# Performance work log

Measured on AMD Instinct MI355X. Metric: run time of the kernel, lower is better.

## Reference

```python
import jax, jax.numpy as jnp
import numpy as np

B, N, C = 1, 6400, 256
NUM_CAMS, NUM_HEADS, NUM_LEVELS, NUM_POINTS = 6, 8, 3, 8
LVL_SHAPES = [(64, 176), (32, 88), (16, 44)]
IMG_H, IMG_W = 512, 1408


def setup_inputs():
    key = jax.random.key(0)
    ks = jax.random.split(key, 16)
    # Gaussian means in ego frame: depth z in [2,40]; x/y scaled so projections land in-image
    z = jax.random.uniform(ks[0], (B, N, 1), minval=2.0, maxval=40.0)
    xy = jax.random.uniform(ks[1], (B, N, 2), minval=-0.5, maxval=0.5)
    means = jnp.concatenate([xy[..., 0:1] * z * 0.8, xy[..., 1:2] * z * 0.4, z], -1)
    feature = jax.random.normal(ks[2], (B, N, C)) * 0.5
    feat0 = jax.random.normal(ks[3], (B * NUM_CAMS, C, 64, 176)) * 0.5
    feat1 = jax.random.normal(ks[4], (B * NUM_CAMS, C, 32, 88)) * 0.5
    feat2 = jax.random.normal(ks[5], (B * NUM_CAMS, C, 16, 44)) * 0.5
    cam2ego = jnp.tile(jnp.eye(4), (B, NUM_CAMS, 1, 1))
    cam2ego = cam2ego.at[..., :3, 3].set(jax.random.uniform(ks[6], (B, NUM_CAMS, 3), minval=-0.5, maxval=0.5))
    intrins = jnp.tile(jnp.array([[500., 0., 704.], [0., 500., 256.], [0., 0., 1.]]), (B, NUM_CAMS, 1, 1))
    post_rots = jnp.tile(jnp.eye(3), (B, NUM_CAMS, 1, 1))
    post_trans = jnp.concatenate([jax.random.uniform(ks[7], (B, NUM_CAMS, 2), minval=-30., maxval=30.),
                                  jnp.zeros((B, NUM_CAMS, 1))], -1)
    # deformable-attn style bias init for sampling offsets (as in init_weights)
    thetas = np.arange(NUM_HEADS) * (2.0 * np.pi / NUM_HEADS)
    grid = np.stack([np.cos(thetas), np.sin(thetas)], -1)
    grid = grid / np.abs(grid).max(-1, keepdims=True)
    grid = np.tile(grid.reshape(NUM_HEADS, 1, 1, 2), (1, NUM_LEVELS, NUM_POINTS, 1))
    grid = grid * (np.arange(NUM_POINTS) + 1).reshape(1, 1, NUM_POINTS, 1)
    b_off = jnp.asarray(grid.reshape(-1), jnp.float32)
    W_off = jax.random.normal(ks[8], (C, NUM_HEADS * NUM_LEVELS * NUM_POINTS * 2)) * 0.01
    W_attn = jax.random.normal(ks[9], (C, NUM_HEADS * NUM_LEVELS * NUM_POINTS)) * 0.02
    b_attn = jnp.zeros((NUM_HEADS * NUM_LEVELS * NUM_POINTS,))
    W_val = jax.random.normal(ks[10], (C, C)) * (1.0 / np.sqrt(C))
    b_val = jnp.zeros((C,))
    W_out = jax.random.normal(ks[11], (C, C)) * (1.0 / np.sqrt(C))
    b_out = jnp.zeros((C,))
    cams_embeds = jax.random.normal(ks[12], (NUM_CAMS, C))
    level_embeds = jax.random.normal(ks[13], (NUM_LEVELS, C))
    ln_g = jnp.ones((C,))
    ln_b = jnp.zeros((C,))
    return dict(means=means, feature=feature, feat0=feat0, feat1=feat1, feat2=feat2,
                cam2ego=cam2ego, intrins=intrins, post_rots=post_rots, post_trans=post_trans,
                W_off=W_off, b_off=b_off, W_attn=W_attn, b_attn=b_attn, W_val=W_val, b_val=b_val,
                W_out=W_out, b_out=b_out, cams_embeds=cams_embeds, level_embeds=level_embeds,
                ln_g=ln_g, ln_b=ln_b, img_h=IMG_H, img_w=IMG_W)


def _msda(value, shapes, loc, attn):
    # Multi-scale deformable attention (matches multi_scale_deformable_attn_pytorch,
    # i.e. grid_sample bilinear, align_corners=False, zero padding).
    # value [Bc,S,H,D]; loc [Bc,Nq,H,L,P,2] in [0,1]; attn [Bc,Nq,H,L,P]
    Bc, S, Hh, D = value.shape
    Nq, P = loc.shape[1], loc.shape[4]
    out = jnp.zeros((Bc, Hh, Nq, D), value.dtype)
    start = 0
    for lvl, (h, w) in enumerate(shapes):
        v = value[:, start:start + h * w].transpose(0, 2, 1, 3)  # [Bc,H,h*w,D]
        l = loc[:, :, :, lvl]                                    # [Bc,Nq,H,P,2]
        x = l[..., 0] * w - 0.5  # align_corners=False pixel coords
        y = l[..., 1] * h - 0.5
        x0 = jnp.floor(x)
        y0 = jnp.floor(y)
        tx = x - x0
        ty = y - y0
        a = attn[:, :, :, lvl]                                   # [Bc,Nq,H,P]
        def samp(xi, yi, wgt):
            valid = (xi >= 0) & (xi <= w - 1) & (yi >= 0) & (yi <= h - 1)
            idx = (jnp.clip(yi, 0, h - 1) * w + jnp.clip(xi, 0, w - 1)).astype(jnp.int32)
            idx = idx.transpose(0, 2, 1, 3).reshape(Bc, Hh, Nq * P)
            g = jnp.take_along_axis(v, idx[..., None], axis=2)   # [Bc,H,Nq*P,D]
            coef = wgt * jnp.where(valid, 1.0, 0.0).astype(v.dtype) * a
            return g * coef.transpose(0, 2, 1, 3).reshape(Bc, Hh, Nq * P, 1)
        acc = (samp(x0, y0, (1 - tx) * (1 - ty)) + samp(x0 + 1, y0, tx * (1 - ty))
               + samp(x0, y0 + 1, (1 - tx) * ty) + samp(x0 + 1, y0 + 1, tx * ty))
        out = out + acc.reshape(Bc, Hh, Nq, P, D).sum(3)
        start += h * w
    return out.transpose(0, 2, 1, 3).reshape(Bc, Nq, Hh * D)


def reference(means, feature, feat0, feat1, feat2, cam2ego, intrins, post_rots, post_trans,
              W_off, b_off, W_attn, b_attn, W_val, b_val, W_out, b_out,
              cams_embeds, level_embeds, ln_g, ln_b, img_h, img_w):
    Bq, Nq, Cc = feature.shape
    D = Cc // NUM_HEADS
    # --- project reference points into each camera (project_reference_points) ---
    mh = jnp.concatenate([means, jnp.ones((Bq, Nq, 1), means.dtype)], -1)      # [B,N,4]
    means_cam = jnp.einsum('bcij,bnj->bcni', jnp.linalg.inv(cam2ego), mh)[..., :3]
    means_img = jnp.einsum('bcij,bcnj->bcni', intrins, means_cam)              # [B,cams,N,3]
    mi = jnp.concatenate([means_img[..., :2] / (means_img[..., 2:] + 1e-4), means_img[..., 2:]], -1)
    mi = jnp.einsum('bcij,bcnj->bcni', post_rots, mi) + post_trans[:, :, None, :]
    coor = mi[..., :2] / jnp.array([img_w, img_h], feature.dtype)              # [B,cams,N,2]
    depth = mi[..., 2]
    mask = ((depth > 0.01) & (coor[..., 0] > 0.) & (coor[..., 0] < 1.)
            & (coor[..., 1] > 0.) & (coor[..., 1] < 1.))                        # [B,cams,N]
    # --- per-query sampling offsets / attention weights (shared across cameras) ---
    offsets = (feature @ W_off + b_off).reshape(Bq, Nq, NUM_HEADS, NUM_LEVELS, NUM_POINTS, 2)
    attn = jax.nn.softmax((feature @ W_attn + b_attn).reshape(Bq, Nq, NUM_HEADS, NUM_LEVELS * NUM_POINTS), -1)
    attn = attn.reshape(Bq, Nq, NUM_HEADS, NUM_LEVELS, NUM_POINTS)
    # --- flatten multi-level feats + cam/level embeds, value projection ---
    feats = (feat0, feat1, feat2)
    shapes = [(f.shape[2], f.shape[3]) for f in feats]
    flat = []
    for lvl, f in enumerate(feats):
        h, w = shapes[lvl]
        fl = f.reshape(Bq, NUM_CAMS, Cc, h * w)
        fl = fl + cams_embeds[None, :, :, None] + level_embeds[lvl][None, None, :, None]
        flat.append(fl)
    value = jnp.concatenate(flat, -1).transpose(0, 1, 3, 2).reshape(Bq * NUM_CAMS, -1, Cc)
    value = (value @ W_val + b_val).reshape(Bq * NUM_CAMS, -1, NUM_HEADS, D)
    # --- sampling locations per camera ---
    norm = jnp.array([[w, h] for (h, w) in shapes], feature.dtype)             # [L,2] = (W_l,H_l)
    loc = coor[:, :, :, None, None, None, :] + offsets[:, None] / norm[None, None, None, None, :, None, :]
    loc = loc.reshape(Bq * NUM_CAMS, Nq, NUM_HEADS, NUM_LEVELS, NUM_POINTS, 2)
    attn_bc = jnp.broadcast_to(attn[:, None], (Bq, NUM_CAMS, Nq, NUM_HEADS, NUM_LEVELS, NUM_POINTS))
    attn_bc = attn_bc.reshape(Bq * NUM_CAMS, Nq, NUM_HEADS, NUM_LEVELS, NUM_POINTS)
    out = _msda(value, shapes, loc, attn_bc).reshape(Bq, NUM_CAMS, Nq, Cc)
    # --- mask-weighted combine over cameras (mathematically equals the rebatch/scatter) ---
    mf = mask.astype(feature.dtype)
    slots = (out * mf[..., None]).sum(1) / jnp.maximum(mf.sum(1), 1.0)[..., None]
    slots = slots @ W_out + b_out
    x = slots + feature  # dropout is identity at inference
    mu = jnp.mean(x, -1, keepdims=True)
    var = jnp.mean((x - mu) ** 2, -1, keepdims=True)
    return (x - mu) / jnp.sqrt(var + 1e-5) * ln_g + ln_b
```

## Files before the change

### kernel.cpp

```cpp
#include <hip/hip_runtime.h>
#include <hip/hip_bf16.h>

typedef __bf16 bf16;
typedef __attribute__((ext_vector_type(4))) float f32x4;
typedef __attribute__((ext_vector_type(8))) bf16 bf16x8;
typedef __attribute__((ext_vector_type(2))) bf16 bf16x2;

#define NCAMS 6
#define NQ 6400
#define CH 256
#define NH 8
#define NL 3
#define NP 8
#define S_TOT 14784

#if __has_builtin(__builtin_amdgcn_fdot2_f32_bf16) && __has_builtin(__builtin_amdgcn_perm)
#define MSDA_DOT2 1
#else
#define MSDA_DOT2 0
#endif

__global__ __launch_bounds__(256) void k_prep(
    const float* __restrict__ means, const float* __restrict__ cam2ego,
    const float* __restrict__ intrins, const float* __restrict__ post_rots,
    const float* __restrict__ post_trans, const int* __restrict__ img_h,
    const int* __restrict__ img_w,
    const float* __restrict__ W_val, const float* __restrict__ W_off,
    const float* __restrict__ W_attn, const float* __restrict__ W_out,
    float* __restrict__ coor, float* __restrict__ maskf,
    bf16* __restrict__ Wvp, bf16* __restrict__ Woap, bf16* __restrict__ Wop)
{
    int bid = blockIdx.x;
    if (bid < 150) {
        int idx = bid * 256 + threadIdx.x;
        if (idx >= NCAMS * NQ) return;
        int cam = idx / NQ, n = idx % NQ;
        float mx = means[n*3+0], my = means[n*3+1], mz = means[n*3+2];
        const float* M = cam2ego + cam*16;
        float R[3][3], t[3];
        #pragma unroll
        for (int r = 0; r < 3; r++) {
            #pragma unroll
            for (int c = 0; c < 3; c++) R[r][c] = M[r*4+c];
            t[r] = M[r*4+3];
        }
        float dx = mx - t[0], dy = my - t[1], dz = mz - t[2];
        float xc = R[0][0]*dx + R[1][0]*dy + R[2][0]*dz;
        float yc = R[0][1]*dx + R[1][1]*dy + R[2][1]*dz;
        float zc = R[0][2]*dx + R[1][2]*dy + R[2][2]*dz;
        const float* K = intrins + cam*9;
        float ix = K[0]*xc + K[1]*yc + K[2]*zc;
        float iy = K[3]*xc + K[4]*yc + K[5]*zc;
        float iz = K[6]*xc + K[7]*yc + K[8]*zc;
        float px = ix / (iz + 1e-4f), py = iy / (iz + 1e-4f), pz = iz;
        const float* P = post_rots + cam*9;
        const float* T = post_trans + cam*3;
        float vx = P[0]*px + P[1]*py + P[2]*pz + T[0];
        float vy = P[3]*px + P[4]*py + P[5]*pz + T[1];
        float vz = P[6]*px + P[7]*py + P[8]*pz + T[2];
        float cx = vx / (float)img_w[0];
        float cy = vy / (float)img_h[0];
        bool ok = (vz > 0.01f) && (cx > 0.f) && (cx < 1.f) && (cy > 0.f) && (cy < 1.f);
        coor[idx*2+0] = cx;
        coor[idx*2+1] = cy;
        maskf[idx] = ok ? 1.f : 0.f;
        return;
    }
    int flat = (bid - 150) * 256 + threadIdx.x;
    if (flat < 8192) {
        int kc = flat >> 10, rem = flat & 1023;
        int nf = rem >> 6, lane = rem & 63;
        int q = lane >> 4, col = nf*16 + (lane & 15);
        bf16x8 v;
        #pragma unroll
        for (int j = 0; j < 8; j++) v[j] = (bf16)W_val[(size_t)(kc*32 + q*8 + j)*256 + col];
        *reinterpret_cast<bf16x8*>(Wvp + (size_t)flat*8) = v;
    } else if (flat < 26624) {
        int f2 = flat - 8192;
        int kc = f2 / (36*64), rem = f2 % (36*64);
        int nf = rem >> 6, lane = rem & 63;
        int q = lane >> 4, col = nf*16 + (lane & 15);
        bf16x8 v;
        #pragma unroll
        for (int j = 0; j < 8; j++) {
            int k = kc*32 + q*8 + j;
            float x = (col < 384) ? W_off[(size_t)k*384 + col] : W_attn[(size_t)k*192 + (col-384)];
            v[j] = (bf16)x;
        }
        *reinterpret_cast<bf16x8*>(Woap + (size_t)f2*8) = v;
    } else if (flat < 34816) {
        int f3 = flat - 26624;
        int kc = f3 >> 10, rem = f3 & 1023;
        int nf = rem >> 6, lane = rem & 63;
        int q = lane >> 4, col = nf*16 + (lane & 15);
        bf16x8 v;
        #pragma unroll
        for (int j = 0; j < 8; j++) v[j] = (bf16)W_out[(size_t)(kc*32 + q*8 + j)*256 + col];
        *reinterpret_cast<bf16x8*>(Wop + (size_t)f3*8) = v;
    }
}

__global__ __launch_bounds__(256) void k_mid(
    const float* __restrict__ feature, const bf16* __restrict__ Woap,
    const float* __restrict__ b_off, const float* __restrict__ b_attn,
    float* __restrict__ offs, bf16* __restrict__ attn_out,
    const float* __restrict__ f0, const float* __restrict__ f1, const float* __restrict__ f2,
    const float* __restrict__ cams_embeds, const float* __restrict__ level_embeds,
    const bf16* __restrict__ Wvp, const float* __restrict__ b_val, bf16* __restrict__ value)
{
    __shared__ alignas(16) char smem[14336];
    int t = threadIdx.x, lane = t & 63, w = t >> 6;
    int q = lane >> 4, r16 = lane & 15;

    if (blockIdx.x < 400) {
        float (*lg)[200] = reinterpret_cast<float(*)[200]>(smem);
        int n0 = blockIdx.x * 16;

        f32x4 acc[9];
        #pragma unroll
        for (int i = 0; i < 9; i++) acc[i] = (f32x4){0.f,0.f,0.f,0.f};

        const float* arow = feature + (size_t)(n0 + r16)*CH;
        for (int kc = 0; kc < 8; kc++) {
            f32x4 a0 = *reinterpret_cast<const f32x4*>(arow + kc*32 + q*8);
            f32x4 a1 = *reinterpret_cast<const f32x4*>(arow + kc*32 + q*8 + 4);
            bf16x8 afr;
            #pragma unroll
            for (int i = 0; i < 4; i++) { afr[i] = (bf16)a0[i]; afr[4+i] = (bf16)a1[i]; }
            #pragma unroll
            for (int nf9 = 0; nf9 < 9; nf9++) {
                bf16x8 bfr = *reinterpret_cast<const bf16x8*>(Woap + ((size_t)(kc*36 + w*9 + nf9)*64 + lane)*8);
                acc[nf9] = __builtin_amdgcn_mfma_f32_16x16x32_bf16(afr, bfr, acc[nf9], 0, 0, 0);
            }
        }
        #pragma unroll
        for (int nf9 = 0; nf9 < 9; nf9++) {
            int nfg = w*9 + nf9;
            int nglob = nfg*16 + r16;
            if (nfg < 24) {
                float bias = b_off[nglob];
                #pragma unroll
                for (int r = 0; r < 4; r++)
                    offs[(size_t)(n0 + q*4 + r)*384 + nglob] = acc[nf9][r] + bias;
            } else {
                int la = nglob - 384;
                float bias = b_attn[la];
                #pragma unroll
                for (int r = 0; r < 4; r++)
                    lg[q*4 + r][la] = acc[nf9][r] + bias;
            }
        }
        __syncthreads();
        if (t < 128) {
            int m = t >> 3, h = t & 7;
            const float* L = &lg[m][h*24];
            float mx = -1e30f;
            #pragma unroll
            for (int j = 0; j < 24; j++) mx = fmaxf(mx, L[j]);
            float e[24]; float s = 0.f;
            #pragma unroll
            for (int j = 0; j < 24; j++) { e[j] = __expf(L[j] - mx); s += e[j]; }
            float inv = 1.f / s;
            #pragma unroll
            for (int j = 0; j < 24; j++) attn_out[(size_t)(n0+m)*192 + h*24 + j] = (bf16)(e[j]*inv);
        }
        return;
    }

    bf16 (*A)[48]    = reinterpret_cast<bf16(*)[48]>(smem);
    bf16 (*Cst)[256] = reinterpret_cast<bf16(*)[256]>(smem + 6144);
    int bi = blockIdx.x - 400;
    int cam = bi / 231, mb = bi % 231;
    int lvl, local0, HW;
    const float* fp;
    if (mb < 176)      { lvl = 0; local0 = mb*64;        fp = f0; HW = 11264; }
    else if (mb < 220) { lvl = 1; local0 = (mb-176)*64;  fp = f1; HW = 2816;  }
    else               { lvl = 2; local0 = (mb-220)*64;  fp = f2; HW = 704;   }
    int pos0 = (lvl == 0 ? 0 : (lvl == 1 ? 11264 : 14080)) + local0;
    const float* featbase = fp + (size_t)cam*CH*HW + local0;

    int kk = t >> 3;
    int m8 = (t & 7) * 8;

    f32x4 acc[4][4];
    #pragma unroll
    for (int i = 0; i < 4; i++)
        #pragma unroll
        for (int j = 0; j < 4; j++) acc[i][j] = (f32x4){0.f,0.f,0.f,0.f};

    for (int kc = 0; kc < 8; kc++) {
        __syncthreads();
        int kg = kc*32 + kk;
        float e = cams_embeds[cam*CH + kg] + level_embeds[lvl*CH + kg];
        f32x4 v0 = *reinterpret_cast<const f32x4*>(featbase + (size_t)kg*HW + m8);
        f32x4 v1 = *reinterpret_cast<const f32x4*>(featbase + (size_t)kg*HW + m8 + 4);
        #pragma unroll
        for (int i = 0; i < 4; i++) A[m8+i][kk]   = (bf16)(v0[i] + e);
        #pragma unroll
        for (int i = 0; i < 4; i++) A[m8+4+i][kk] = (bf16)(v1[i] + e);
        __syncthreads();

        bf16x8 bfr[4];
        #pragma unroll
        for (int nf = 0; nf < 4; nf++) {
            int nfg = w*4 + nf;
            bfr[nf] = *reinterpret_cast<const bf16x8*>(Wvp + ((size_t)(kc*16 + nfg)*64 + lane)*8);
        }
        #pragma unroll
        for (int mf = 0; mf < 4; mf++) {
            bf16x8 afr = *reinterpret_cast<const bf16x8*>(&A[mf*16 + r16][q*8]);
            #pragma unroll
            for (int nf = 0; nf < 4; nf++)
                acc[mf][nf] = __builtin_amdgcn_mfma_f32_16x16x32_bf16(afr, bfr[nf], acc[mf][nf], 0, 0, 0);
        }
    }
    int orow = t >> 4;
    int ocol = (t & 15) * 16;
    int ohead = ocol >> 5, och = ocol & 31;
    #pragma unroll
    for (int mf = 0; mf < 4; mf++) {
        __syncthreads();
        #pragma unroll
        for (int nf = 0; nf < 4; nf++) {
            int c = w*64 + nf*16 + r16;
            float bv = b_val[c];
            #pragma unroll
            for (int r = 0; r < 4; r++)
                Cst[q*4 + r][c] = (bf16)(acc[mf][nf][r] + bv);
        }
        __syncthreads();
        int srow = pos0 + mf*16 + orow;
        bf16* dst = value + ((size_t)(cam*NH + ohead)*S_TOT + srow)*32 + och;
        const f32x4* src = reinterpret_cast<const f32x4*>(&Cst[orow][ocol]);
        f32x4 x0 = src[0], x1 = src[1];
        reinterpret_cast<f32x4*>(dst)[0] = x0;
        reinterpret_cast<f32x4*>(dst)[1] = x1;
    }
}

__global__ __launch_bounds__(256) void k_msda(
    const float* __restrict__ coor, const float* __restrict__ offs,
    const bf16* __restrict__ attn, const bf16* __restrict__ value,
    const float* __restrict__ maskf, float* __restrict__ slots)
{
    __shared__ int4  s_o[NCAMS*192];
#if MSDA_DOT2
    __shared__ uint2 s_w[NCAMS*192];
#else
    __shared__ f32x4 s_w[NCAMS*192];
#endif
    int n = blockIdx.x;
    int t = threadIdx.x;

    for (int it = t; it < NCAMS*192; it += 256) {
        int cam = it / 192;
        int r   = it - cam*192;
        int hh  = r / 24;
        int rr  = r - hh*24;
        int lvl = rr >> 3;

        float mk = maskf[cam*NQ + n];
        float cx = coor[(cam*NQ + n)*2 + 0];
        float cy = coor[(cam*NQ + n)*2 + 1];
        float2 o2 = *reinterpret_cast<const float2*>(offs + (size_t)n*384 + r*2);
        float aw = (float)attn[(size_t)n*192 + r] * mk;

        int wi   = (lvl == 0) ? 176 : ((lvl == 1) ? 88 : 44);
        int hi   = (lvl == 0) ? 64  : ((lvl == 1) ? 32 : 16);
        int base = (lvl == 0) ? 0   : ((lvl == 1) ? 11264 : 14080);

        float x = cx*(float)wi + o2.x - 0.5f;
        float y = cy*(float)hi + o2.y - 0.5f;
        float xf = floorf(x), yf = floorf(y);
        float tx = x - xf, ty = y - yf;
        float wm1x = (float)(wi-1), wm1y = (float)(hi-1);
        bool vx0 = (xf >= 0.f)      && (xf <= wm1x);
        bool vx1 = (xf+1.f >= 0.f)  && (xf+1.f <= wm1x);
        bool vy0 = (yf >= 0.f)      && (yf <= wm1y);
        bool vy1 = (yf+1.f >= 0.f)  && (yf+1.f <= wm1y);
        int x0 = (int)fminf(fmaxf(xf,      0.f), wm1x);
        int x1 = (int)fminf(fmaxf(xf+1.f,  0.f), wm1x);
        int y0 = (int)fminf(fmaxf(yf,      0.f), wm1y);
        int y1 = (int)fminf(fmaxf(yf+1.f,  0.f), wm1y);
        float w00 = (1.f-tx)*(1.f-ty)*aw * ((vx0 && vy0) ? 1.f : 0.f);
        float w10 = tx*(1.f-ty)*aw       * ((vx1 && vy0) ? 1.f : 0.f);
        float w01 = (1.f-tx)*ty*aw       * ((vx0 && vy1) ? 1.f : 0.f);
        float w11 = tx*ty*aw             * ((vx1 && vy1) ? 1.f : 0.f);
        int rowb = (cam*NH + hh)*S_TOT + base;
        int r0 = rowb + y0*wi, r1 = rowb + y1*wi;
        s_o[it] = make_int4((r0 + x0)*64, (r0 + x1)*64, (r1 + x0)*64, (r1 + x1)*64);
#if MSDA_DOT2
        bf16x2 wa; wa[0] = (bf16)w00; wa[1] = (bf16)w10;
        bf16x2 wb; wb[0] = (bf16)w01; wb[1] = (bf16)w11;
        s_w[it] = make_uint2(__builtin_bit_cast(unsigned, wa),
                             __builtin_bit_cast(unsigned, wb));
#else
        s_w[it] = (f32x4){w00, w10, w01, w11};
#endif
    }
    __syncthreads();

    int lane = t & 63, wv = t >> 6;
    int hl = lane >> 5;
    int p  = (lane >> 2) & 7;
    int k2 = lane & 3;
    int hglob = wv*2 + hl;
    int kb = k2 * 16;
    int ibase = hglob*24 + p;

    f32x4 acc0 = (f32x4){0.f,0.f,0.f,0.f};
    f32x4 acc1 = (f32x4){0.f,0.f,0.f,0.f};
    const char* vbyte = (const char*)value;

    uint4 cA0,cA1,cA2, cB0,cB1,cB2, cC0,cC1,cC2, cD0,cD1,cD2;
#if MSDA_DOT2
    uint2 cw0, cw1, cw2;
#else
    f32x4 cw0, cw1, cw2;
#endif

#define LOADBATCH(CAMIDX, A0,A1,A2, B0,B1,B2, C0,C1,C2, D0,D1,D2, W0,W1,W2) \
    { int itb = (CAMIDX)*192 + ibase; \
      int4 o0 = s_o[itb]; int4 o1 = s_o[itb+8]; int4 o2v = s_o[itb+16]; \
      A0 = *reinterpret_cast<const uint4*>(vbyte + (o0.x + kb)); \
      B0 = *reinterpret_cast<const uint4*>(vbyte + (o0.y + kb)); \
      C0 = *reinterpret_cast<const uint4*>(vbyte + (o0.z + kb)); \
      D0 = *reinterpret_cast<const uint4*>(vbyte + (o0.w + kb)); \
      A1 = *reinterpret_cast<const uint4*>(vbyte + (o1.x + kb)); \
      B1 = *reinterpret_cast<const uint4*>(vbyte + (o1.y + kb)); \
      C1 = *reinterpret_cast<const uint4*>(vbyte + (o1.z + kb)); \
      D1 = *reinterpret_cast<const uint4*>(vbyte + (o1.w + kb)); \
      A2 = *reinterpret_cast<const uint4*>(vbyte + (o2v.x + kb)); \
      B2 = *reinterpret_cast<const uint4*>(vbyte + (o2v.y + kb)); \
      C2 = *reinterpret_cast<const uint4*>(vbyte + (o2v.z + kb)); \
      D2 = *reinterpret_cast<const uint4*>(vbyte + (o2v.w + kb)); \
      W0 = s_w[itb]; W1 = s_w[itb+8]; W2 = s_w[itb+16]; }

#if MSDA_DOT2
#define CONSUME1(d00, d10, d01, d11, WP) \
    { bf16x2 wa = __builtin_bit_cast(bf16x2, (WP).x); \
      bf16x2 wb = __builtin_bit_cast(bf16x2, (WP).y); \
      unsigned a0 = __builtin_amdgcn_perm((d10).x, (d00).x, 0x05040100u); \
      unsigned a1 = __builtin_amdgcn_perm((d10).x, (d00).x, 0x07060302u); \
      unsigned a2 = __builtin_amdgcn_perm((d10).y, (d00).y, 0x05040100u); \
      unsigned a3 = __builtin_amdgcn_perm((d10).y, (d00).y, 0x07060302u); \
      unsigned a4 = __builtin_amdgcn_perm((d10).z, (d00).z, 0x05040100u); \
      unsigned a5 = __builtin_amdgcn_perm((d10).z, (d00).z, 0x07060302u); \
      unsigned a6 = __builtin_amdgcn_perm((d10).w, (d00).w, 0x05040100u); \
      unsigned a7 = __builtin_amdgcn_perm((d10).w, (d00).w, 0x07060302u); \
      acc0[0] = __builtin_amdgcn_fdot2_f32_bf16(__builtin_bit_cast(bf16x2, a0), wa, acc0[0], false); \
      acc0[1] = __builtin_amdgcn_fdot2_f32_bf16(__builtin_bit_cast(bf16x2, a1), wa, acc0[1], false); \
      acc0[2] = __builtin_amdgcn_fdot2_f32_bf16(__builtin_bit_cast(bf16x2, a2), wa, acc0[2], false); \
      acc0[3] = __builtin_amdgcn_fdot2_f32_bf16(__builtin_bit_cast(bf16x2, a3), wa, acc0[3], false); \
      acc1[0] = __builtin_amdgcn_fdot2_f32_bf16(__builtin_bit_cast(bf16x2, a4), wa, acc1[0], false); \
      acc1[1] = __builtin_amdgcn_fdot2_f32_bf16(__builtin_bit_cast(bf16x2, a5), wa, acc1[1], false); \
      acc1[2] = __builtin_amdgcn_fdot2_f32_bf16(__builtin_bit_cast(bf16x2, a6), wa, acc1[2], false); \
      acc1[3] = __builtin_amdgcn_fdot2_f32_bf16(__builtin_bit_cast(bf16x2, a7), wa, acc1[3], false); \
      unsigned b0 = __builtin_amdgcn_perm((d11).x, (d01).x, 0x05040100u); \
      unsigned b1 = __builtin_amdgcn_perm((d11).x, (d01).x, 0x07060302u); \
      unsigned b2 = __builtin_amdgcn_perm((d11).y, (d01).y, 0x05040100u); \
      unsigned b3 = __builtin_amdgcn_perm((d11).y, (d01).y, 0x07060302u); \
      unsigned b4 = __builtin_amdgcn_perm((d11).z, (d01).z, 0x05040100u); \
      unsigned b5 = __builtin_amdgcn_perm((d11).z, (d01).z, 0x07060302u); \
      unsigned b6 = __builtin_amdgcn_perm((d11).w, (d01).w, 0x05040100u); \
      unsigned b7 = __builtin_amdgcn_perm((d11).w, (d01).w, 0x07060302u); \
      acc0[0] = __builtin_amdgcn_fdot2_f32_bf16(__builtin_bit_cast(bf16x2, b0), wb, acc0[0], false); \
      acc0[1] = __builtin_amdgcn_fdot2_f32_bf16(__builtin_bit_cast(bf16x2, b1), wb, acc0[1], false); \
      acc0[2] = __builtin_amdgcn_fdot2_f32_bf16(__builtin_bit_cast(bf16x2, b2), wb, acc0[2], false); \
      acc0[3] = __builtin_amdgcn_fdot2_f32_bf16(__builtin_bit_cast(bf16x2, b3), wb, acc0[3], false); \
      acc1[0] = __builtin_amdgcn_fdot2_f32_bf16(__builtin_bit_cast(bf16x2, b4), wb, acc1[0], false); \
      acc1[1] = __builtin_amdgcn_fdot2_f32_bf16(__builtin_bit_cast(bf16x2, b5), wb, acc1[1], false); \
      acc1[2] = __builtin_amdgcn_fdot2_f32_bf16(__builtin_bit_cast(bf16x2, b6), wb, acc1[2], false); \
      acc1[3] = __builtin_amdgcn_fdot2_f32_bf16(__builtin_bit_cast(bf16x2, b7), wb, acc1[3], false); }
#else
#define CONSUME1(d00, d10, d01, d11, WP) \
    { f32x4 w4 = (WP); \
      acc0[0] = fmaf(__uint_as_float((d00).x << 16),         w4.x, acc0[0]); \
      acc0[1] = fmaf(__uint_as_float((d00).x & 0xffff0000u), w4.x, acc0[1]); \
      acc0[2] = fmaf(__uint_as_float((d00).y << 16),         w4.x, acc0[2]); \
      acc0[3] = fmaf(__uint_as_float((d00).y & 0xffff0000u), w4.x, acc0[3]); \
      acc1[0] = fmaf(__uint_as_float((d00).z << 16),         w4.x, acc1[0]); \
      acc1[1] = fmaf(__uint_as_float((d00).z & 0xffff0000u), w4.x, acc1[1]); \
      acc1[2] = fmaf(__uint_as_float((d00).w << 16),         w4.x, acc1[2]); \
      acc1[3] = fmaf(__uint_as_float((d00).w & 0xffff0000u), w4.x, acc1[3]); \
      acc0[0] = fmaf(__uint_as_float((d10).x << 16),         w4.y, acc0[0]); \
      acc0[1] = fmaf(__uint_as_float((d10).x & 0xffff0000u), w4.y, acc0[1]); \
      acc0[2] = fmaf(__uint_as_float((d10).y << 16),         w4.y, acc0[2]); \
      acc0[3] = fmaf(__uint_as_float((d10).y & 0xffff0000u), w4.y, acc0[3]); \
      acc1[0] = fmaf(__uint_as_float((d10).z << 16),         w4.y, acc1[0]); \
      acc1[1] = fmaf(__uint_as_float((d10).z & 0xffff0000u), w4.y, acc1[1]); \
      acc1[2] = fmaf(__uint_as_float((d10).w << 16),         w4.y, acc1[2]); \
      acc1[3] = fmaf(__uint_as_float((d10).w & 0xffff0000u), w4.y, acc1[3]); \
      acc0[0] = fmaf(__uint_as_float((d01).x << 16),         w4.z, acc0[0]); \
      acc0[1] = fmaf(__uint_as_float((d01).x & 0xffff0000u), w4.z, acc0[1]); \
      acc0[2] = fmaf(__uint_as_float((d01).y << 16),         w4.z, acc0[2]); \
      acc0[3] = fmaf(__uint_as_float((d01).y & 0xffff0000u), w4.z, acc0[3]); \
      acc1[0] = fmaf(__uint_as_float((d01).z << 16),         w4.z, acc1[0]); \
      acc1[1] = fmaf(__uint_as_float((d01).z & 0xffff0000u), w4.z, acc1[1]); \
      acc1[2] = fmaf(__uint_as_float((d01).w << 16),         w4.z, acc1[2]); \
      acc1[3] = fmaf(__uint_as_float((d01).w & 0xffff0000u), w4.z, acc1[3]); \
      acc0[0] = fmaf(__uint_as_float((d11).x << 16),         w4.w, acc0[0]); \
      acc0[1] = fmaf(__uint_as_float((d11).x & 0xffff0000u), w4.w, acc0[1]); \
      acc0[2] = fmaf(__uint_as_float((d11).y << 16),         w4.w, acc0[2]); \
      acc0[3] = fmaf(__uint_as_float((d11).y & 0xffff0000u), w4.w, acc0[3]); \
      acc1[0] = fmaf(__uint_as_float((d11).z << 16),         w4.w, acc1[0]); \
      acc1[1] = fmaf(__uint_as_float((d11).z & 0xffff0000u), w4.w, acc1[1]); \
      acc1[2] = fmaf(__uint_as_float((d11).w << 16),         w4.w, acc1[2]); \
      acc1[3] = fmaf(__uint_as_float((d11).w & 0xffff0000u), w4.w, acc1[3]); }
#endif

    LOADBATCH(0, cA0,cA1,cA2, cB0,cB1,cB2, cC0,cC1,cC2, cD0,cD1,cD2, cw0,cw1,cw2)

    #pragma unroll
    for (int cam = 0; cam < NCAMS; cam++) {
        uint4 nA0,nA1,nA2, nB0,nB1,nB2, nC0,nC1,nC2, nD0,nD1,nD2;
#if MSDA_DOT2
        uint2 nw0, nw1, nw2;
#else
        f32x4 nw0, nw1, nw2;
#endif
        if (cam + 1 < NCAMS) {
            LOADBATCH(cam+1, nA0,nA1,nA2, nB0,nB1,nB2, nC0,nC1,nC2, nD0,nD1,nD2, nw0,nw1,nw2)
        }
        CONSUME1(cA0, cB0, cC0, cD0, cw0)
        CONSUME1(cA1, cB1, cC1, cD1, cw1)
        CONSUME1(cA2, cB2, cC2, cD2, cw2)
        if (cam + 1 < NCAMS) {
            cA0=nA0; cA1=nA1; cA2=nA2; cB0=nB0; cB1=nB1; cB2=nB2;
            cC0=nC0; cC1=nC1; cC2=nC2; cD0=nD0; cD1=nD1; cD2=nD2;
            cw0=nw0; cw1=nw1; cw2=nw2;
        }
    }
#undef LOADBATCH
#undef CONSUME1

    #pragma unroll
    for (int i = 0; i < 4; i++) {
        acc0[i] += __shfl_xor(acc0[i], 4);
        acc0[i] += __shfl_xor(acc0[i], 8);
        acc0[i] += __shfl_xor(acc0[i], 16);
        acc1[i] += __shfl_xor(acc1[i], 4);
        acc1[i] += __shfl_xor(acc1[i], 8);
        acc1[i] += __shfl_xor(acc1[i], 16);
    }
    if (p == 0) {
        float* dst = slots + (size_t)n*CH + hglob*32 + k2*8;
        *reinterpret_cast<f32x4*>(dst)     = acc0;
        *reinterpret_cast<f32x4*>(dst + 4) = acc1;
    }
}

__global__ __launch_bounds__(256) void k_final2(
    const float* __restrict__ slots, const float* __restrict__ maskf,
    const bf16* __restrict__ Wop, const float* __restrict__ b_out,
    const float* __restrict__ feature, const float* __restrict__ ln_g,
    const float* __restrict__ ln_b, float* __restrict__ out)
{
    __shared__ float yb[16][264];
    int t = threadIdx.x, lane = t & 63, w = t >> 6;
    int q = lane >> 4, r16 = lane & 15;
    int n0 = blockIdx.x * 16;

    float msum = 0.f;
    #pragma unroll
    for (int cam = 0; cam < NCAMS; cam++) msum += maskf[cam*NQ + n0 + r16];
    float inv = 1.f / fmaxf(msum, 1.f);

    f32x4 acc[4];
    #pragma unroll
    for (int i = 0; i < 4; i++) acc[i] = (f32x4){0.f,0.f,0.f,0.f};

    const float* srow = slots + (size_t)(n0 + r16)*CH;
    for (int kc = 0; kc < 8; kc++) {
        f32x4 a0 = *reinterpret_cast<const f32x4*>(srow + kc*32 + q*8);
        f32x4 a1 = *reinterpret_cast<const f32x4*>(srow + kc*32 + q*8 + 4);
        bf16x8 afr;
        #pragma unroll
        for (int i = 0; i < 4; i++) { afr[i] = (bf16)(a0[i]*inv); afr[4+i] = (bf16)(a1[i]*inv); }
        #pragma unroll
        for (int nf = 0; nf < 4; nf++) {
            bf16x8 bfr = *reinterpret_cast<const bf16x8*>(Wop + ((size_t)(kc*16 + w*4 + nf)*64 + lane)*8);
            acc[nf] = __builtin_amdgcn_mfma_f32_16x16x32_bf16(afr, bfr, acc[nf], 0, 0, 0);
        }
    }
    #pragma unroll
    for (int nf = 0; nf < 4; nf++) {
        int c = (w*4 + nf)*16 + r16;
        float bias = b_out[c];
        #pragma unroll
        for (int r = 0; r < 4; r++) {
            int m = q*4 + r;
            yb[m][c] = acc[nf][r] + bias + feature[(size_t)(n0+m)*CH + c];
        }
    }
    __syncthreads();
    int row = t >> 4, l16 = t & 15;
    int c0 = l16 * 16;
    float s = 0.f, s2 = 0.f;
    #pragma unroll
    for (int j = 0; j < 16; j++) {
        float v = yb[row][c0 + j];
        s += v; s2 += v*v;
    }
    #pragma unroll
    for (int off = 1; off < 16; off <<= 1) {
        s  += __shfl_xor(s, off);
        s2 += __shfl_xor(s2, off);
    }
    float mu = s / 256.f;
    float rsig = rsqrtf(s2 / 256.f - mu*mu + 1e-5f);
    float* orow = out + (size_t)(n0 + row)*CH + c0;
    #pragma unroll
    for (int j4 = 0; j4 < 4; j4++) {
        f32x4 o;
        #pragma unroll
        for (int i = 0; i < 4; i++) {
            int c = c0 + j4*4 + i;
            o[i] = (yb[row][c] - mu) * rsig * ln_g[c] + ln_b[c];
        }
        *reinterpret_cast<f32x4*>(orow + j4*4) = o;
    }
}

extern "C" void kernel_launch(void* const* d_in, const int* in_sizes, int n_in,
                              void* d_out, int out_size, void* d_ws, size_t ws_size,
                              hipStream_t stream)
{
    const float* means       = (const float*)d_in[0];
    const float* feature     = (const float*)d_in[1];
    const float* feat0       = (const float*)d_in[2];
    const float* feat1       = (const float*)d_in[3];
    const float* feat2       = (const float*)d_in[4];
    const float* cam2ego     = (const float*)d_in[5];
    const float* intrins     = (const float*)d_in[6];
    const float* post_rots   = (const float*)d_in[7];
    const float* post_trans  = (const float*)d_in[8];
    const float* W_off       = (const float*)d_in[9];
    const float* b_off       = (const float*)d_in[10];
    const float* W_attn      = (const float*)d_in[11];
    const float* b_attn      = (const float*)d_in[12];
    const float* W_val       = (const float*)d_in[13];
    const float* b_val       = (const float*)d_in[14];
    const float* W_out       = (const float*)d_in[15];
    const float* b_out       = (const float*)d_in[16];
    const float* cams_embeds = (const float*)d_in[17];
    const float* level_embeds= (const float*)d_in[18];
    const float* ln_g        = (const float*)d_in[19];
    const float* ln_b        = (const float*)d_in[20];
    const int*   img_h       = (const int*)d_in[21];
    const int*   img_w       = (const int*)d_in[22];

    char* ws = (char*)d_ws;
    float* coor  = (float*)(ws + 0);
    float* maskf = (float*)(ws + 307200);
    float* offs  = (float*)(ws + 460800);
    bf16*  attn  = (bf16*) (ws + 10291200);
    bf16*  Wvp   = (bf16*) (ws + 12748800);
    bf16*  Woap  = (bf16*) (ws + 12879872);
    bf16*  Wop   = (bf16*) (ws + 13174784);
    float* slots = (float*)(ws + 13305856);
    bf16*  value = (bf16*) (ws + 19859456);
    if (ws_size < 65275904u) return;

    k_prep  <<<286, 256, 0, stream>>>(means, cam2ego, intrins, post_rots, post_trans,
                                      img_h, img_w, W_val, W_off, W_attn, W_out,
                                      coor, maskf, Wvp, Woap, Wop);
    k_mid   <<<1786, 256, 0, stream>>>(feature, Woap, b_off, b_attn, offs, attn,
                                       feat0, feat1, feat2, cams_embeds, level_embeds,
                                       Wvp, b_val, value);
    k_msda  <<<6400, 256, 0, stream>>>(coor, offs, attn, value, maskf, slots);
    k_final2<<<400, 256, 0, stream>>>(slots, maskf, Wop, b_out, feature, ln_g, ln_b, (float*)d_out);
}
```

Before: 308.4 us.

## Split mid kernel, pack MSDA offsets, hand-schedule gather loads with waitcnt

Splits the combined offset/attention and value-projection kernel into two separate launches. In the sampling kernel, the four per-corner offsets shrink to two ints, with the x-step encoded in a low bit. The value gathers are issued as inline-asm global_load_dwordx4 with explicit vmcnt waits and a sched barrier, so the next camera's loads stay in flight while the current one is consumed. The trade-off is an extra kernel launch, and manual waitcnt counting that can break if the compiler inserts other memory ops.

```diff
diff --git a/kernel.cpp b/kernel.cpp
--- a/kernel.cpp
+++ b/kernel.cpp
@@ -5,6 +5,7 @@
 typedef __attribute__((ext_vector_type(4))) float f32x4;
 typedef __attribute__((ext_vector_type(8))) bf16 bf16x8;
 typedef __attribute__((ext_vector_type(2))) bf16 bf16x2;
+typedef __attribute__((ext_vector_type(4))) unsigned int u32x4;
 
 #define NCAMS 6
 #define NQ 6400
@@ -100,76 +101,74 @@
     }
 }
 
-__global__ __launch_bounds__(256) void k_mid(
+__global__ __launch_bounds__(256) void k_offattn2(
     const float* __restrict__ feature, const bf16* __restrict__ Woap,
     const float* __restrict__ b_off, const float* __restrict__ b_attn,
-    float* __restrict__ offs, bf16* __restrict__ attn_out,
+    float* __restrict__ offs, bf16* __restrict__ attn_out)
+{
+    __shared__ float lg[16][200];
+    int t = threadIdx.x, lane = t & 63, w = t >> 6;
+    int q = lane >> 4, r16 = lane & 15;
+    int n0 = blockIdx.x * 16;
+
+    f32x4 acc[9];
+    #pragma unroll
+    for (int i = 0; i < 9; i++) acc[i] = (f32x4){0.f,0.f,0.f,0.f};
+
+    const float* arow = feature + (size_t)(n0 + r16)*CH;
+    for (int kc = 0; kc < 8; kc++) {
+        f32x4 a0 = *reinterpret_cast<const f32x4*>(arow + kc*32 + q*8);
+        f32x4 a1 = *reinterpret_cast<const f32x4*>(arow + kc*32 + q*8 + 4);
+        bf16x8 afr;
+        #pragma unroll
+        for (int i = 0; i < 4; i++) { afr[i] = (bf16)a0[i]; afr[4+i] = (bf16)a1[i]; }
+        #pragma unroll
+        for (int nf9 = 0; nf9 < 9; nf9++) {
+            bf16x8 bfr = *reinterpret_cast<const bf16x8*>(Woap + ((size_t)(kc*36 + w*9 + nf9)*64 + lane)*8);
+            acc[nf9] = __builtin_amdgcn_mfma_f32_16x16x32_bf16(afr, bfr, acc[nf9], 0, 0, 0);
+        }
+    }
+    #pragma unroll
+    for (int nf9 = 0; nf9 < 9; nf9++) {
+        int nfg = w*9 + nf9;
+        int nglob = nfg*16 + r16;
+        if (nfg < 24) {
+            float bias = b_off[nglob];
+            #pragma unroll
+            for (int r = 0; r < 4; r++)
+                offs[(size_t)(n0 + q*4 + r)*384 + nglob] = acc[nf9][r] + bias;
+        } else {
+            int la = nglob - 384;
+            float bias = b_attn[la];
+            #pragma unroll
+            for (int r = 0; r < 4; r++)
+                lg[q*4 + r][la] = acc[nf9][r] + bias;
+        }
+    }
+    __syncthreads();
+    if (t < 128) {
+        int m = t >> 3, h = t & 7;
+        const float* L = &lg[m][h*24];
+        float mx = -1e30f;
+        #pragma unroll
+        for (int j = 0; j < 24; j++) mx = fmaxf(mx, L[j]);
+        float e[24]; float s = 0.f;
+        #pragma unroll
+        for (int j = 0; j < 24; j++) { e[j] = __expf(L[j] - mx); s += e[j]; }
+        float inv = 1.f / s;
+        #pragma unroll
+        for (int j = 0; j < 24; j++) attn_out[(size_t)(n0+m)*192 + h*24 + j] = (bf16)(e[j]*inv);
+    }
+}
+
+__global__ __launch_bounds__(256) void k_valproj(
     const float* __restrict__ f0, const float* __restrict__ f1, const float* __restrict__ f2,
     const float* __restrict__ cams_embeds, const float* __restrict__ level_embeds,
     const bf16* __restrict__ Wvp, const float* __restrict__ b_val, bf16* __restrict__ value)
 {
-    __shared__ alignas(16) char smem[14336];
-    int t = threadIdx.x, lane = t & 63, w = t >> 6;
-    int q = lane >> 4, r16 = lane & 15;
-
-    if (blockIdx.x < 400) {
-        float (*lg)[200] = reinterpret_cast<float(*)[200]>(smem);
-        int n0 = blockIdx.x * 16;
-
-        f32x4 acc[9];
-        #pragma unroll
-        for (int i = 0; i < 9; i++) acc[i] = (f32x4){0.f,0.f,0.f,0.f};
-
-        const float* arow = feature + (size_t)(n0 + r16)*CH;
-        for (int kc = 0; kc < 8; kc++) {
-            f32x4 a0 = *reinterpret_cast<const f32x4*>(arow + kc*32 + q*8);
-            f32x4 a1 = *reinterpret_cast<const f32x4*>(arow + kc*32 + q*8 + 4);
-            bf16x8 afr;
-            #pragma unroll
-            for (int i = 0; i < 4; i++) { afr[i] = (bf16)a0[i]; afr[4+i] = (bf16)a1[i]; }
-            #pragma unroll
-            for (int nf9 = 0; nf9 < 9; nf9++) {
-                bf16x8 bfr = *reinterpret_cast<const bf16x8*>(Woap + ((size_t)(kc*36 + w*9 + nf9)*64 + lane)*8);
-                acc[nf9] = __builtin_amdgcn_mfma_f32_16x16x32_bf16(afr, bfr, acc[nf9], 0, 0, 0);
-            }
-        }
-        #pragma unroll
-        for (int nf9 = 0; nf9 < 9; nf9++) {
-            int nfg = w*9 + nf9;
-            int nglob = nfg*16 + r16;
-            if (nfg < 24) {
-                float bias = b_off[nglob];
-                #pragma unroll
-                for (int r = 0; r < 4; r++)
-                    offs[(size_t)(n0 + q*4 + r)*384 + nglob] = acc[nf9][r] + bias;
-            } else {
-                int la = nglob - 384;
-                float bias = b_attn[la];
-                #pragma unroll
-                for (int r = 0; r < 4; r++)
-                    lg[q*4 + r][la] = acc[nf9][r] + bias;
-            }
-        }
-        __syncthreads();
-        if (t < 128) {
-            int m = t >> 3, h = t & 7;
-            const float* L = &lg[m][h*24];
-            float mx = -1e30f;
-            #pragma unroll
-            for (int j = 0; j < 24; j++) mx = fmaxf(mx, L[j]);
-            float e[24]; float s = 0.f;
-            #pragma unroll
-            for (int j = 0; j < 24; j++) { e[j] = __expf(L[j] - mx); s += e[j]; }
-            float inv = 1.f / s;
-            #pragma unroll
-            for (int j = 0; j < 24; j++) attn_out[(size_t)(n0+m)*192 + h*24 + j] = (bf16)(e[j]*inv);
-        }
-        return;
-    }
-
-    bf16 (*A)[48]    = reinterpret_cast<bf16(*)[48]>(smem);
-    bf16 (*Cst)[256] = reinterpret_cast<bf16(*)[256]>(smem + 6144);
-    int bi = blockIdx.x - 400;
+    __shared__ alignas(16) bf16 A[64][48];
+    __shared__ alignas(16) bf16 Cst[16][256];
+    int bi = blockIdx.x;
     int cam = bi / 231, mb = bi % 231;
     int lvl, local0, HW;
     const float* fp;
@@ -179,8 +178,11 @@
     int pos0 = (lvl == 0 ? 0 : (lvl == 1 ? 11264 : 14080)) + local0;
     const float* featbase = fp + (size_t)cam*CH*HW + local0;
 
+    int t = threadIdx.x;
+    int lane = t & 63, w = t >> 6;
     int kk = t >> 3;
     int m8 = (t & 7) * 8;
+    int q = lane >> 4, r16 = lane & 15;
 
     f32x4 acc[4][4];
     #pragma unroll
@@ -243,7 +245,7 @@
     const bf16* __restrict__ attn, const bf16* __restrict__ value,
     const float* __restrict__ maskf, float* __restrict__ slots)
 {
-    __shared__ int4  s_o[NCAMS*192];
+    __shared__ int2  s_o[NCAMS*192];
 #if MSDA_DOT2
     __shared__ uint2 s_w[NCAMS*192];
 #else
@@ -288,7 +290,7 @@
         float w11 = tx*ty*aw             * ((vx1 && vy1) ? 1.f : 0.f);
         int rowb = (cam*NH + hh)*S_TOT + base;
         int r0 = rowb + y0*wi, r1 = rowb + y1*wi;
-        s_o[it] = make_int4((r0 + x0)*64, (r0 + x1)*64, (r1 + x0)*64, (r1 + x1)*64);
+        s_o[it] = make_int2((r0 + x0)*64 + (x1 - x0), (r1 + x0)*64);
 #if MSDA_DOT2
         bf16x2 wa; wa[0] = (bf16)w00; wa[1] = (bf16)w10;
         bf16x2 wb; wb[0] = (bf16)w01; wb[1] = (bf16)w11;
@@ -312,42 +314,43 @@
     f32x4 acc1 = (f32x4){0.f,0.f,0.f,0.f};
     const char* vbyte = (const char*)value;
 
-    uint4 cA0,cA1,cA2, cB0,cB1,cB2, cC0,cC1,cC2, cD0,cD1,cD2;
+    u32x4 cA0,cB0,cC0,cD0, cA1,cB1,cC1,cD1, cA2,cB2,cC2,cD2;
+    u32x4 nA0,nB0,nC0,nD0, nA1,nB1,nC1,nD1, nA2,nB2,nC2,nD2;
 #if MSDA_DOT2
-    uint2 cw0, cw1, cw2;
+    uint2 cw0,cw1,cw2, nw0,nw1,nw2;
 #else
-    f32x4 cw0, cw1, cw2;
+    f32x4 cw0,cw1,cw2, nw0,nw1,nw2;
 #endif
 
-#define LOADBATCH(CAMIDX, A0,A1,A2, B0,B1,B2, C0,C1,C2, D0,D1,D2, W0,W1,W2) \
-    { int itb = (CAMIDX)*192 + ibase; \
-      int4 o0 = s_o[itb]; int4 o1 = s_o[itb+8]; int4 o2v = s_o[itb+16]; \
-      A0 = *reinterpret_cast<const uint4*>(vbyte + (o0.x + kb)); \
-      B0 = *reinterpret_cast<const uint4*>(vbyte + (o0.y + kb)); \
-      C0 = *reinterpret_cast<const uint4*>(vbyte + (o0.z + kb)); \
-      D0 = *reinterpret_cast<const uint4*>(vbyte + (o0.w + kb)); \
-      A1 = *reinterpret_cast<const uint4*>(vbyte + (o1.x + kb)); \
-      B1 = *reinterpret_cast<const uint4*>(vbyte + (o1.y + kb)); \
-      C1 = *reinterpret_cast<const uint4*>(vbyte + (o1.z + kb)); \
-      D1 = *reinterpret_cast<const uint4*>(vbyte + (o1.w + kb)); \
-      A2 = *reinterpret_cast<const uint4*>(vbyte + (o2v.x + kb)); \
-      B2 = *reinterpret_cast<const uint4*>(vbyte + (o2v.y + kb)); \
-      C2 = *reinterpret_cast<const uint4*>(vbyte + (o2v.z + kb)); \
-      D2 = *reinterpret_cast<const uint4*>(vbyte + (o2v.w + kb)); \
-      W0 = s_w[itb]; W1 = s_w[itb+8]; W2 = s_w[itb+16]; }
+#define GLD(dst, ptr) \
+    asm volatile("global_load_dwordx4 %0, %1, off" : "=v"(dst) : "v"(ptr))
+
+#define ISSUECAM(CI, A0,B0,C0,D0, A1,B1,C1,D1, A2,B2,C2,D2, W0,W1,W2) { \
+    int itb = (CI)*192 + ibase; \
+    int2 o0 = s_o[itb]; int2 o1 = s_o[itb+8]; int2 o2v = s_o[itb+16]; \
+    W0 = s_w[itb]; W1 = s_w[itb+8]; W2 = s_w[itb+16]; \
+    { int sb = o0.x & 1; int dxb = sb << 6; \
+      const char* pa = vbyte + (o0.x - sb) + kb; const char* pc = vbyte + o0.y + kb; \
+      GLD(A0, pa); GLD(B0, pa + dxb); GLD(C0, pc); GLD(D0, pc + dxb); } \
+    { int sb = o1.x & 1; int dxb = sb << 6; \
+      const char* pa = vbyte + (o1.x - sb) + kb; const char* pc = vbyte + o1.y + kb; \
+      GLD(A1, pa); GLD(B1, pa + dxb); GLD(C1, pc); GLD(D1, pc + dxb); } \
+    { int sb = o2v.x & 1; int dxb = sb << 6; \
+      const char* pa = vbyte + (o2v.x - sb) + kb; const char* pc = vbyte + o2v.y + kb; \
+      GLD(A2, pa); GLD(B2, pa + dxb); GLD(C2, pc); GLD(D2, pc + dxb); } }
 
 #if MSDA_DOT2
 #define CONSUME1(d00, d10, d01, d11, WP) \
     { bf16x2 wa = __builtin_bit_cast(bf16x2, (WP).x); \
       bf16x2 wb = __builtin_bit_cast(bf16x2, (WP).y); \
-      unsigned a0 = __builtin_amdgcn_perm((d10).x, (d00).x, 0x05040100u); \
-      unsigned a1 = __builtin_amdgcn_perm((d10).x, (d00).x, 0x07060302u); \
-      unsigned a2 = __builtin_amdgcn_perm((d10).y, (d00).y, 0x05040100u); \
-      unsigned a3 = __builtin_amdgcn_perm((d10).y, (d00).y, 0x07060302u); \
-      unsigned a4 = __builtin_amdgcn_perm((d10).z, (d00).z, 0x05040100u); \
-      unsigned a5 = __builtin_amdgcn_perm((d10).z, (d00).z, 0x07060302u); \
-      unsigned a6 = __builtin_amdgcn_perm((d10).w, (d00).w, 0x05040100u); \
-      unsigned a7 = __builtin_amdgcn_perm((d10).w, (d00).w, 0x07060302u); \
+      unsigned a0 = __builtin_amdgcn_perm((d10)[0], (d00)[0], 0x05040100u); \
+      unsigned a1 = __builtin_amdgcn_perm((d10)[0], (d00)[0], 0x07060302u); \
+      unsigned a2 = __builtin_amdgcn_perm((d10)[1], (d00)[1], 0x05040100u); \
+      unsigned a3 = __builtin_amdgcn_perm((d10)[1], (d00)[1], 0x07060302u); \
+      unsigned a4 = __builtin_amdgcn_perm((d10)[2], (d00)[2], 0x05040100u); \
+      unsigned a5 = __builtin_amdgcn_perm((d10)[2], (d00)[2], 0x07060302u); \
+      unsigned a6 = __builtin_amdgcn_perm((d10)[3], (d00)[3], 0x05040100u); \
+      unsigned a7 = __builtin_amdgcn_perm((d10)[3], (d00)[3], 0x07060302u); \
       acc0[0] = __builtin_amdgcn_fdot2_f32_bf16(__builtin_bit_cast(bf16x2, a0), wa, acc0[0], false); \
       acc0[1] = __builtin_amdgcn_fdot2_f32_bf16(__builtin_bit_cast(bf16x2, a1), wa, acc0[1], false); \
       acc0[2] = __builtin_amdgcn_fdot2_f32_bf16(__builtin_bit_cast(bf16x2, a2), wa, acc0[2], false); \
@@ -356,14 +359,14 @@
       acc1[1] = __builtin_amdgcn_fdot2_f32_bf16(__builtin_bit_cast(bf16x2, a5), wa, acc1[1], false); \
       acc1[2] = __builtin_amdgcn_fdot2_f32_bf16(__builtin_bit_cast(bf16x2, a6), wa, acc1[2], false); \
       acc1[3] = __builtin_amdgcn_fdot2_f32_bf16(__builtin_bit_cast(bf16x2, a7), wa, acc1[3], false); \
-      unsigned b0 = __builtin_amdgcn_perm((d11).x, (d01).x, 0x05040100u); \
-      unsigned b1 = __builtin_amdgcn_perm((d11).x, (d01).x, 0x07060302u); \
-      unsigned b2 = __builtin_amdgcn_perm((d11).y, (d01).y, 0x05040100u); \
-      unsigned b3 = __builtin_amdgcn_perm((d11).y, (d01).y, 0x07060302u); \
-      unsigned b4 = __builtin_amdgcn_perm((d11).z, (d01).z, 0x05040100u); \
-      unsigned b5 = __builtin_amdgcn_perm((d11).z, (d01).z, 0x07060302u); \
-      unsigned b6 = __builtin_amdgcn_perm((d11).w, (d01).w, 0x05040100u); \
-      unsigned b7 = __builtin_amdgcn_perm((d11).w, (d01).w, 0x07060302u); \
+      unsigned b0 = __builtin_amdgcn_perm((d11)[0], (d01)[0], 0x05040100u); \
+      unsigned b1 = __builtin_amdgcn_perm((d11)[0], (d01)[0], 0x07060302u); \
+      unsigned b2 = __builtin_amdgcn_perm((d11)[1], (d01)[1], 0x05040100u); \
+      unsigned b3 = __builtin_amdgcn_perm((d11)[1], (d01)[1], 0x07060302u); \
+      unsigned b4 = __builtin_amdgcn_perm((d11)[2], (d01)[2], 0x05040100u); \
+      unsigned b5 = __builtin_amdgcn_perm((d11)[2], (d01)[2], 0x07060302u); \
+      unsigned b6 = __builtin_amdgcn_perm((d11)[3], (d01)[3], 0x05040100u); \
+      unsigned b7 = __builtin_amdgcn_perm((d11)[3], (d01)[3], 0x07060302u); \
       acc0[0] = __builtin_amdgcn_fdot2_f32_bf16(__builtin_bit_cast(bf16x2, b0), wb, acc0[0], false); \
       acc0[1] = __builtin_amdgcn_fdot2_f32_bf16(__builtin_bit_cast(bf16x2, b1), wb, acc0[1], false); \
       acc0[2] = __builtin_amdgcn_fdot2_f32_bf16(__builtin_bit_cast(bf16x2, b2), wb, acc0[2], false); \
@@ -375,63 +378,63 @@
 #else
 #define CONSUME1(d00, d10, d01, d11, WP) \
     { f32x4 w4 = (WP); \
-      acc0[0] = fmaf(__uint_as_float((d00).x << 16),         w4.x, acc0[0]); \
-      acc0[1] = fmaf(__uint_as_float((d00).x & 0xffff0000u), w4.x, acc0[1]); \
-      acc0[2] = fmaf(__uint_as_float((d00).y << 16),         w4.x, acc0[2]); \
-      acc0[3] = fmaf(__uint_as_float((d00).y & 0xffff0000u), w4.x, acc0[3]); \
-      acc1[0] = fmaf(__uint_as_float((d00).z << 16),         w4.x, acc1[0]); \
-      acc1[1] = fmaf(__uint_as_float((d00).z & 0xffff0000u), w4.x, acc1[1]); \
-      acc1[2] = fmaf(__uint_as_float((d00).w << 16),         w4.x, acc1[2]); \
-      acc1[3] = fmaf(__uint_as_float((d00).w & 0xffff0000u), w4.x, acc1[3]); \
-      acc0[0] = fmaf(__uint_as_float((d10).x << 16),         w4.y, acc0[0]); \
-      acc0[1] = fmaf(__uint_as_float((d10).x & 0xffff0000u), w4.y, acc0[1]); \
-      acc0[2] = fmaf(__uint_as_float((d10).y << 16),         w4.y, acc0[2]); \
-      acc0[3] = fmaf(__uint_as_float((d10).y & 0xffff0000u), w4.y, acc0[3]); \
-      acc1[0] = fmaf(__uint_as_float((d10).z << 16),         w4.y, acc1[0]); \
-      acc1[1] = fmaf(__uint_as_float((d10).z & 0xffff0000u), w4.y, acc1[1]); \
-      acc1[2] = fmaf(__uint_as_float((d10).w << 16),         w4.y, acc1[2]); \
-      acc1[3] = fmaf(__uint_as_float((d10).w & 0xffff0000u), w4.y, acc1[3]); \
-      acc0[0] = fmaf(__uint_as_float((d01).x << 16),         w4.z, acc0[0]); \
-      acc0[1] = fmaf(__uint_as_float((d01).x & 0xffff0000u), w4.z, acc0[1]); \
-      acc0[2] = fmaf(__uint_as_float((d01).y << 16),         w4.z, acc0[2]); \
-      acc0[3] = fmaf(__uint_as_float((d01).y & 0xffff0000u), w4.z, acc0[3]); \
-      acc1[0] = fmaf(__uint_as_float((d01).z << 16),         w4.z, acc1[0]); \
-      acc1[1] = fmaf(__uint_as_float((d01).z & 0xffff0000u), w4.z, acc1[1]); \
-      acc1[2] = fmaf(__uint_as_float((d01).w << 16),         w4.z, acc1[2]); \
-      acc1[3] = fmaf(__uint_as_float((d01).w & 0xffff0000u), w4.z, acc1[3]); \
-      acc0[0] = fmaf(__uint_as_float((d11).x << 16),         w4.w, acc0[0]); \
-      acc0[1] = fmaf(__uint_as_float((d11).x & 0xffff0000u), w4.w, acc0[1]); \
-      acc0[2] = fmaf(__uint_as_float((d11).y << 16),         w4.w, acc0[2]); \
-      acc0[3] = fmaf(__uint_as_float((d11).y & 0xffff0000u), w4.w, acc0[3]); \
-      acc1[0] = fmaf(__uint_as_float((d11).z << 16),         w4.w, acc1[0]); \
-      acc1[1] = fmaf(__uint_as_float((d11).z & 0xffff0000u), w4.w, acc1[1]); \
-      acc1[2] = fmaf(__uint_as_float((d11).w << 16),         w4.w, acc1[2]); \
-      acc1[3] = fmaf(__uint_as_float((d11).w & 0xffff0000u), w4.w, acc1[3]); }
+      acc0[0] = fmaf(__uint_as_float((d00)[0] << 16),         w4.x, acc0[0]); \
+      acc0[1] = fmaf(__uint_as_float((d00)[0] & 0xffff0000u), w4.x, acc0[1]); \
+      acc0[2] = fmaf(__uint_as_float((d00)[1] << 16),         w4.x, acc0[2]); \
+      acc0[3] = fmaf(__uint_as_float((d00)[1] & 0xffff0000u), w4.x, acc0[3]); \
+      acc1[0] = fmaf(__uint_as_float((d00)[2] << 16),         w4.x, acc1[0]); \
+      acc1[1] = fmaf(__uint_as_float((d00)[2] & 0xffff0000u), w4.x, acc1[1]); \
+      acc1[2] = fmaf(__uint_as_float((d00)[3] << 16),         w4.x, acc1[2]); \
+      acc1[3] = fmaf(__uint_as_float((d00)[3] & 0xffff0000u), w4.x, acc1[3]); \
+      acc0[0] = fmaf(__uint_as_float((d10)[0] << 16),         w4.y, acc0[0]); \
+      acc0[1] = fmaf(__uint_as_float((d10)[0] & 0xffff0000u), w4.y, acc0[1]); \
+      acc0[2] = fmaf(__uint_as_float((d10)[1] << 16),         w4.y, acc0[2]); \
+      acc0[3] = fmaf(__uint_as_float((d10)[1] & 0xffff0000u), w4.y, acc0[3]); \
+      acc1[0] = fmaf(__uint_as_float((d10)[2] << 16),         w4.y, acc1[0]); \
+      acc1[1] = fmaf(__uint_as_float((d10)[2] & 0xffff0000u), w4.y, acc1[1]); \
+      acc1[2] = fmaf(__uint_as_float((d10)[3] << 16),         w4.y, acc1[2]); \
+      acc1[3] = fmaf(__uint_as_float((d10)[3] & 0xffff0000u), w4.y, acc1[3]); \
+      acc0[0] = fmaf(__uint_as_float((d01)[0] << 16),         w4.z, acc0[0]); \
+      acc0[1] = fmaf(__uint_as_float((d01)[0] & 0xffff0000u), w4.z, acc0[1]); \
+      acc0[2] = fmaf(__uint_as_float((d01)[1] << 16),         w4.z, acc0[2]); \
+      acc0[3] = fmaf(__uint_as_float((d01)[1] & 0xffff0000u), w4.z, acc0[3]); \
+      acc1[0] = fmaf(__uint_as_float((d01)[2] << 16),         w4.z, acc1[0]); \
+      acc1[1] = fmaf(__uint_as_float((d01)[2] & 0xffff0000u), w4.z, acc1[1]); \
+      acc1[2] = fmaf(__uint_as_float((d01)[3] << 16),         w4.z, acc1[2]); \
+      acc1[3] = fmaf(__uint_as_float((d01)[3] & 0xffff0000u), w4.z, acc1[3]); \
+      acc0[0] = fmaf(__uint_as_float((d11)[0] << 16),         w4.w, acc0[0]); \
+      acc0[1] = fmaf(__uint_as_float((d11)[0] & 0xffff0000u), w4.w, acc0[1]); \
+      acc0[2] = fmaf(__uint_as_float((d11)[1] << 16),         w4.w, acc0[2]); \
+      acc0[3] = fmaf(__uint_as_float((d11)[1] & 0xffff0000u), w4.w, acc0[3]); \
+      acc1[0] = fmaf(__uint_as_float((d11)[2] << 16),         w4.w, acc1[0]); \
+      acc1[1] = fmaf(__uint_as_float((d11)[2] & 0xffff0000u), w4.w, acc1[1]); \
+      acc1[2] = fmaf(__uint_as_float((d11)[3] << 16),         w4.w, acc1[2]); \
+      acc1[3] = fmaf(__uint_as_float((d11)[3] & 0xffff0000u), w4.w, acc1[3]); }
 #endif
 
-    LOADBATCH(0, cA0,cA1,cA2, cB0,cB1,cB2, cC0,cC1,cC2, cD0,cD1,cD2, cw0,cw1,cw2)
+    ISSUECAM(0, cA0,cB0,cC0,cD0, cA1,cB1,cC1,cD1, cA2,cB2,cC2,cD2, cw0,cw1,cw2)
 
     #pragma unroll
     for (int cam = 0; cam < NCAMS; cam++) {
-        uint4 nA0,nA1,nA2, nB0,nB1,nB2, nC0,nC1,nC2, nD0,nD1,nD2;
-#if MSDA_DOT2
-        uint2 nw0, nw1, nw2;
-#else
-        f32x4 nw0, nw1, nw2;
-#endif
         if (cam + 1 < NCAMS) {
-            LOADBATCH(cam+1, nA0,nA1,nA2, nB0,nB1,nB2, nC0,nC1,nC2, nD0,nD1,nD2, nw0,nw1,nw2)
-        }
+            ISSUECAM(cam+1, nA0,nB0,nC0,nD0, nA1,nB1,nC1,nD1, nA2,nB2,nC2,nD2, nw0,nw1,nw2)
+            asm volatile("s_waitcnt vmcnt(12)" ::: "memory");
+        } else {
+            asm volatile("s_waitcnt vmcnt(0)" ::: "memory");
+        }
+        __builtin_amdgcn_sched_barrier(0);
         CONSUME1(cA0, cB0, cC0, cD0, cw0)
         CONSUME1(cA1, cB1, cC1, cD1, cw1)
         CONSUME1(cA2, cB2, cC2, cD2, cw2)
         if (cam + 1 < NCAMS) {
-            cA0=nA0; cA1=nA1; cA2=nA2; cB0=nB0; cB1=nB1; cB2=nB2;
-            cC0=nC0; cC1=nC1; cC2=nC2; cD0=nD0; cD1=nD1; cD2=nD2;
+            cA0=nA0; cB0=nB0; cC0=nC0; cD0=nD0;
+            cA1=nA1; cB1=nB1; cC1=nC1; cD1=nD1;
+            cA2=nA2; cB2=nB2; cC2=nC2; cD2=nD2;
             cw0=nw0; cw1=nw1; cw2=nw2;
         }
     }
-#undef LOADBATCH
+#undef GLD
+#undef ISSUECAM
 #undef CONSUME1
 
     #pragma unroll
@@ -562,12 +565,11 @@
     bf16*  value = (bf16*) (ws + 19859456);
     if (ws_size < 65275904u) return;
 
-    k_prep  <<<286, 256, 0, stream>>>(means, cam2ego, intrins, post_rots, post_trans,
-                                      img_h, img_w, W_val, W_off, W_attn, W_out,
-                                      coor, maskf, Wvp, Woap, Wop);
-    k_mid   <<<1786, 256, 0, stream>>>(feature, Woap, b_off, b_attn, offs, attn,
-                                       feat0, feat1, feat2, cams_embeds, level_embeds,
-                                       Wvp, b_val, value);
-    k_msda  <<<6400, 256, 0, stream>>>(coor, offs, attn, value, maskf, slots);
-    k_final2<<<400, 256, 0, stream>>>(slots, maskf, Wop, b_out, feature, ln_g, ln_b, (float*)d_out);
+    k_prep    <<<286, 256, 0, stream>>>(means, cam2ego, intrins, post_rots, post_trans,
+                                        img_h, img_w, W_val, W_off, W_attn, W_out,
+                                        coor, maskf, Wvp, Woap, Wop);
+    k_offattn2<<<400, 256, 0, stream>>>(feature, Woap, b_off, b_attn, offs, attn);
+    k_valproj <<<1386, 256, 0, stream>>>(feat0, feat1, feat2, cams_embeds, level_embeds, Wvp, b_val, value);
+    k_msda    <<<6400, 256, 0, stream>>>(coor, offs, attn, value, maskf, slots);
+    k_final2  <<<400, 256, 0, stream>>>(slots, maskf, Wop, b_out, feature, ln_g, ln_b, (float*)d_out);
 }
```

New measurement: 307.7 us. About the same (-0.2%).
